# Optimization experiments

Hardware: AMD Instinct MI355X
Metric: run time of the kernel (lower is better)

Reference implementation:

```python
import jax, jax.numpy as jnp
import numpy as np

B, T, D = 2, 2048, 1024
N, K, H = 16, 8, 128  # q heads, kv heads, head_dim
G = N // K            # GQA group size
EPS = 1e-6
THETA = 1000000.0
SCALE = H ** -0.5
K_MASK = float(np.finfo(np.float32).min)


def rms_norm(x, scale):
    # RMSNorm over head_dim (last axis), computed in fp32 like the original
    dtype = x.dtype
    rms = jnp.sqrt(jnp.mean(x.astype(jnp.float32) ** 2, axis=-1, keepdims=True) + EPS)
    return (scale * x / rms).astype(dtype)


def positions_from_segment_ids(seg):
    t = jnp.arange(seg.shape[1], dtype=jnp.int32)[None, :]
    off = jnp.argmax(seg, axis=1, keepdims=True).astype(jnp.int32)
    rel = t - off
    return jnp.where(seg != 0, rel, jnp.int32(2 ** 30))


def rope_sin_cos(positions):
    frac = jnp.arange(0, H, 2, dtype=jnp.float32) / H
    inv_freq = 1.0 / (THETA ** frac)                    # [H/2]
    ang = positions.astype(jnp.float32)[..., None] * inv_freq  # [B,T,H/2]
    return jnp.sin(ang), jnp.cos(ang)


def apply_rope(x, sin, cos):
    # x: [B,T,heads,H]; sin/cos: [B,T,H/2]
    x1, x2 = x[..., : H // 2], x[..., H // 2:]
    s, c = sin[:, :, None, :], cos[:, :, None, :]
    return jnp.concatenate([x1 * c - x2 * s, x2 * c + x1 * s], axis=-1).astype(x.dtype)


def setup_inputs() -> dict:
    key = jax.random.key(0)
    ks = jax.random.split(key, 8)
    std = 0.02
    return {
        "x": jax.random.normal(ks[0], (B, T, D), dtype=jnp.float32),
        "segment_ids": jnp.ones((B, T), dtype=jnp.int32),
        "wq": jax.random.normal(ks[1], (D, N, H), dtype=jnp.float32) * std,
        "wk": jax.random.normal(ks[2], (D, K, H), dtype=jnp.float32) * std,
        "wv": jax.random.normal(ks[3], (D, K, H), dtype=jnp.float32) * std,
        "wo": jax.random.normal(ks[4], (N, H, D), dtype=jnp.float32) * std,
        "q_scale": jnp.ones((H,), dtype=jnp.float32),
        "k_scale": jnp.ones((H,), dtype=jnp.float32),
    }


def reference(x, segment_ids, wq, wk, wv, wo, q_scale, k_scale):
    # QKV projections + QK RMSNorm
    q = rms_norm(jnp.einsum('BTD,DNH->BTNH', x, wq), q_scale)  # [B,T,N,H]
    k = rms_norm(jnp.einsum('BSD,DKH->BSKH', x, wk), k_scale)  # [B,T,K,H]
    v = jnp.einsum('BSD,DKH->BSKH', x, wv)                     # [B,T,K,H]

    # RoPE using segment-relative positions
    pos = positions_from_segment_ids(segment_ids)  # [B,T] int32
    sin, cos = rope_sin_cos(pos)
    q = apply_rope(q, sin, cos)
    k = apply_rope(k, sin, cos)

    # GQA attention: [B,T,K,G,H] x [B,S,K,H] -> [B,T,S,K,G]
    qg = q.reshape(B, T, K, G, H)
    logits = jnp.einsum('BTKGH,BSKH->BTSKG', qg, k) * SCALE

    causal = pos[:, None, :] <= pos[:, :, None]                       # [B,T,S]
    segm = segment_ids[:, None, :] == segment_ids[:, :, None]         # [B,T,S]
    mask = (causal & segm)[:, :, :, None, None]
    logits = jnp.where(mask, logits, K_MASK)

    w = jax.nn.softmax(logits.astype(jnp.float32), axis=2).astype(logits.dtype)
    out = jnp.einsum('BTSKG,BSKH->BTKGH', w, v).reshape(B, T, N, H)
    return jnp.einsum('BTNH,NHD->BTD', out, wo)
```

## Files before the change

kernel.cpp:

```cpp
#include <hip/hip_runtime.h>
#include <hip/hip_bf16.h>


typedef unsigned short u16;
typedef __attribute__((ext_vector_type(8))) short s16x8;
typedef __attribute__((ext_vector_type(4))) float fp32x4;
typedef __attribute__((ext_vector_type(4))) u16 u16x4;

#define MFMA_BF16(a, b, c) __builtin_amdgcn_mfma_f32_16x16x32_bf16((a), (b), (c), 0, 0, 0)

static constexpr int Bq = 2, Tq = 2048, Dq = 1024, NHq = 16, KHq = 8, Hq = 128;
static constexpr float EPSq = 1e-6f;
static constexpr float S2q = 0.08838834764831845f * 1.4426950408889634f;
static constexpr float MAXq = 20.0f;
static constexpr float NEGHUGE = -3.0e38f;

__device__ __forceinline__ u16 f2b(float f) {
  __hip_bfloat16 h = __float2bfloat16(f);
  return *reinterpret_cast<u16*>(&h);
}

__device__ __forceinline__ void gload16(const u16* g, u16* lds_base) {
  __builtin_amdgcn_global_load_lds(
      (const __attribute__((address_space(1))) unsigned int*)(const void*)g,
      (__attribute__((address_space(3))) unsigned int*)(void*)lds_base, 16, 0, 0);
}


__global__ __launch_bounds__(256) void prep_kernel(
    const float* __restrict__ x, const float* __restrict__ wq,
    const float* __restrict__ wk, const float* __restrict__ wv,
    const float* __restrict__ wo, const int* __restrict__ seg,
    u16* __restrict__ xb, u16* __restrict__ wqkv_t, u16* __restrict__ wo_t,
    int* __restrict__ pos) {
  const int bid = blockIdx.x;
  const int tid = threadIdx.x;
  if (bid < 4096) {
    const int i = bid * 1024 + tid * 4;
    const float4 v = *reinterpret_cast<const float4*>(x + i);
    u16x4 o;
    o.x = f2b(v.x); o.y = f2b(v.y); o.z = f2b(v.z); o.w = f2b(v.w);
    *reinterpret_cast<u16x4*>(xb + i) = o;
    return;
  }
  __shared__ float tile[32][33];
  __shared__ int sv[256], si[256];
  const int tx = tid & 31, ty = tid >> 5;
  if (bid < 8192) {
    const int z = bid - 4096;
    const int r0 = (z & 31) * 32;
    const int c0 = (z >> 5) * 32;
    const float* src;
    int stride, coff;
    if (c0 < 2048)      { src = wq; stride = 2048; coff = c0; }
    else if (c0 < 3072) { src = wk; stride = 1024; coff = c0 - 2048; }
    else                { src = wv; stride = 1024; coff = c0 - 3072; }
#pragma unroll
    for (int j = 0; j < 32; j += 8)
      tile[ty + j][tx] = src[(long)(r0 + ty + j) * stride + (coff + tx)];
    __syncthreads();
#pragma unroll
    for (int j = 0; j < 32; j += 8)
      wqkv_t[(long)(c0 + ty + j) * 1024 + (r0 + tx)] = f2b(tile[tx][ty + j]);
    return;
  }
  if (bid < 10240) {
    const int z = bid - 8192;
    const int c0 = (z & 31) * 32;
    const int r0 = (z >> 5) * 32;
#pragma unroll
    for (int j = 0; j < 32; j += 8)
      tile[ty + j][tx] = wo[(long)(r0 + ty + j) * 1024 + (c0 + tx)];
    __syncthreads();
#pragma unroll
    for (int j = 0; j < 32; j += 8)
      wo_t[(long)(c0 + ty + j) * 2048 + (r0 + tx)] = f2b(tile[tx][ty + j]);
    return;
  }
  const int b = bid - 10240;
  const int* s = seg + b * Tq;
  int bestv = -2147483647 - 1, besti = 0x7fffffff;
  for (int t = tid; t < Tq; t += 256) {
    int v = s[t];
    if (v > bestv) { bestv = v; besti = t; }
  }
  sv[tid] = bestv; si[tid] = besti;
  __syncthreads();
  for (int k = 128; k > 0; k >>= 1) {
    if (tid < k) {
      int v2 = sv[tid + k], i2 = si[tid + k];
      if (v2 > sv[tid] || (v2 == sv[tid] && i2 < si[tid])) {
        sv[tid] = v2; si[tid] = i2;
      }
    }
    __syncthreads();
  }
  const int off = si[0];
  for (int t = tid; t < Tq; t += 256)
    pos[b * Tq + t] = (s[t] != 0) ? (t - off) : (1 << 30);
}


template <typename OutT, int BN>
__global__ __launch_bounds__(256) void gemm_bt_kernel(
    const u16* __restrict__ A, const u16* __restrict__ Bt, OutT* __restrict__ C,
    u16* __restrict__ vtout, int M, int N, int Kd) {
  constexpr int JT = BN / 32;
  __shared__ __align__(16) u16 As[128][64];
  __shared__ __align__(16) u16 Bs[BN][64];
  const int tid = threadIdx.x;
  const int wave = tid >> 6, lane = tid & 63;
  const int quad = lane >> 4, l16 = lane & 15;
  const int m0 = blockIdx.y * 128, n0 = blockIdx.x * BN;
  const int wm = (wave >> 1) * 64, wn = (wave & 1) * (BN / 2);
  const int row8 = lane >> 3;
  const int cgl = (lane & 7) ^ row8;

  const fp32x4 z4 = {0.f, 0.f, 0.f, 0.f};
  fp32x4 acc[4][JT];
#pragma unroll
  for (int i = 0; i < 4; ++i)
#pragma unroll
    for (int j = 0; j < JT; ++j) acc[i][j] = z4;

  for (int k0 = 0; k0 < Kd; k0 += 64) {
    __syncthreads();
#pragma unroll
    for (int jj = 0; jj < 4; ++jj) {
      const int R = wave * 32 + jj * 8;
      gload16(A + (size_t)(m0 + R + row8) * Kd + k0 + cgl * 8, &As[R][0]);
    }
    if constexpr (BN == 128) {
#pragma unroll
      for (int jj = 0; jj < 4; ++jj) {
        const int R = wave * 32 + jj * 8;
        gload16(Bt + (size_t)(n0 + R + row8) * Kd + k0 + cgl * 8, &Bs[R][0]);
      }
    } else {
#pragma unroll
      for (int jj = 0; jj < 2; ++jj) {
        const int R = wave * 16 + jj * 8;
        gload16(Bt + (size_t)(n0 + R + row8) * Kd + k0 + cgl * 8, &Bs[R][0]);
      }
    }
    __syncthreads();
#pragma unroll
    for (int kh = 0; kh < 2; ++kh) {
      s16x8 af[4], bfr[JT];
#pragma unroll
      for (int i = 0; i < 4; ++i)
        af[i] = *(const s16x8*)&As[wm + i * 16 + l16]
                               [((((kh << 2) | quad) ^ (l16 & 7)) << 3)];
#pragma unroll
      for (int j = 0; j < JT; ++j)
        bfr[j] = *(const s16x8*)&Bs[wn + j * 16 + l16]
                                [((((kh << 2) | quad) ^ (l16 & 7)) << 3)];
#pragma unroll
      for (int i = 0; i < 4; ++i)
#pragma unroll
        for (int j = 0; j < JT; ++j) acc[i][j] = MFMA_BF16(af[i], bfr[j], acc[i][j]);
    }
  }

  if constexpr (sizeof(OutT) == 2) {
    if (n0 >= 3072) {
      const int kv8 = (n0 - 3072) >> 7;
      const int bq = m0 >> 11;
      const size_t vbase = (size_t)(bq * KHq + kv8) * Hq * Tq;
#pragma unroll
      for (int i = 0; i < 4; ++i) {
        const int t = (m0 + wm + i * 16 + quad * 4) & 2047;
#pragma unroll
        for (int j = 0; j < JT; ++j) {
          const int h = wn + j * 16 + l16;
          u16x4 o;
#pragma unroll
          for (int r = 0; r < 4; ++r) o[r] = f2b(acc[i][j][r]);
          *reinterpret_cast<u16x4*>(&vtout[vbase + (size_t)h * Tq + t]) = o;
        }
      }
      return;
    }
  }
#pragma unroll
  for (int i = 0; i < 4; ++i) {
    const int row = m0 + wm + i * 16 + quad * 4;
#pragma unroll
    for (int j = 0; j < JT; ++j) {
      const int col = n0 + wn + j * 16 + l16;
#pragma unroll
      for (int r = 0; r < 4; ++r) {
        const float v = acc[i][j][r];
        if constexpr (sizeof(OutT) == 2)
          ((u16*)C)[(size_t)(row + r) * N + col] = f2b(v);
        else
          ((float*)C)[(size_t)(row + r) * N + col] = v;
      }
    }
  }
}


__global__ __launch_bounds__(256) void norm_rope_kernel(
    u16* __restrict__ qkv, const int* __restrict__ pos,
    const float* __restrict__ q_scale, const float* __restrict__ k_scale) {
  const int w = blockIdx.x * 4 + (threadIdx.x >> 6);
  const int lane = threadIdx.x & 63;
  const int bt = w / 24, head = w % 24;
  const bool isq = head < NHq;
  const int col = isq ? head * Hq : 2048 + (head - NHq) * Hq;
  u16* p = qkv + (size_t)bt * 4096 + col;
  const float e1 = (float)*reinterpret_cast<const __hip_bfloat16*>(&p[lane]);
  const float e2 = (float)*reinterpret_cast<const __hip_bfloat16*>(&p[lane + 64]);
  float ss = e1 * e1 + e2 * e2;
#pragma unroll
  for (int d = 1; d < 64; d <<= 1) ss += __shfl_xor(ss, d, 64);
  const float rinv = rsqrtf(ss * (1.0f / 128.0f) + EPSq);
  const float* sc = isq ? q_scale : k_scale;
  const float n1 = sc[lane] * e1 * rinv;
  const float n2 = sc[lane + 64] * e2 * rinv;
  const int P = pos[bt];
  const float inv_freq =
      __builtin_amdgcn_exp2f(-(float)lane * (19.931568569324174f / 64.0f));
  float r = (float)P * inv_freq * 0.15915494309189535f;
  r -= floorf(r);
  const float s = __builtin_amdgcn_sinf(r);
  const float c = __builtin_amdgcn_cosf(r);
  p[lane] = f2b(n1 * c - n2 * s);
  p[lane + 64] = f2b(n2 * c + n1 * s);
}


__global__ __launch_bounds__(256, 2) void flash_kernel(
    const u16* __restrict__ qkv, const u16* __restrict__ vt,
    const int* __restrict__ pos, const int* __restrict__ seg,
    u16* __restrict__ Obuf) {
  const int tid = threadIdx.x;
  const int w = tid >> 6;
  const int lane = tid & 63;
  const int quad = lane >> 4, l16 = lane & 15;
  const int g = blockIdx.x;
  const int b = g & 1;
  const int kv = (g >> 1) & 7;
  const int qh = kv * 2 + ((g >> 4) & 1);
  const int p = g >> 5;

  __shared__ __align__(16) u16 Ks[64][128];
  __shared__ __align__(16) u16 Vs[128][64];
  __shared__ __align__(16) u16 Ps[4][16][72];

  const u16* kbase = qkv + (size_t)(b * Tq) * 4096 + 2048 + kv * Hq;
  const u16* vbase = vt + (size_t)(b * KHq + kv) * Hq * Tq;
  const int krow_off = lane >> 4;
  const int vrow_off = lane >> 3;
  const fp32x4 z4 = {0.f, 0.f, 0.f, 0.f};

#pragma unroll
  for (int phase = 0; phase < 2; ++phase) {
    const int c = phase ? p : 31 - p;
    const int t0 = c * 64 + w * 16;
    const int nst = c + 1;

    s16x8 qf[4];
    {
      const u16* qrow = qkv + (size_t)(b * Tq + t0 + l16) * 4096 + qh * Hq;
#pragma unroll
      for (int ks = 0; ks < 4; ++ks)
        qf[ks] = *(const s16x8*)(qrow + ks * 32 + quad * 8);
    }
    int my_pos[4], my_seg[4];
#pragma unroll
    for (int i = 0; i < 4; ++i) {
      const int t = t0 + quad * 4 + i;
      my_pos[i] = pos[b * Tq + t];
      my_seg[i] = seg[b * Tq + t];
    }
    float l_i[4];
#pragma unroll
    for (int i = 0; i < 4; ++i) l_i[i] = 0.f;
    fp32x4 o_acc[8];
#pragma unroll
    for (int h = 0; h < 8; ++h) o_acc[h] = z4;

    for (int st = 0; st < nst; ++st) {
      const int s0 = st * 64;
      __syncthreads();
#pragma unroll
      for (int j = 0; j < 4; ++j) {
        const int R = w * 16 + j * 4;
        const int r = R + krow_off;
        const int cg = (lane & 15) ^ (r & 15);
        gload16(kbase + (size_t)(s0 + r) * 4096 + cg * 8, &Ks[R][0]);
      }
#pragma unroll
      for (int j = 0; j < 4; ++j) {
        const int R = w * 32 + j * 8;
        const int r = R + vrow_off;
        const int cg = (lane & 7) ^ (vrow_off & 7);
        gload16(vbase + (size_t)r * Tq + s0 + cg * 8, &Vs[R][0]);
      }
      __syncthreads();

      fp32x4 sc[4];
#pragma unroll
      for (int sub = 0; sub < 4; ++sub) sc[sub] = z4;
#pragma unroll
      for (int sub = 0; sub < 4; ++sub)
#pragma unroll
        for (int ks = 0; ks < 4; ++ks) {
          const s16x8 kf =
              *(const s16x8*)&Ks[sub * 16 + l16][((((ks << 2) | quad) ^ l16) << 3)];
          sc[sub] = MFMA_BF16(qf[ks], kf, sc[sub]);
        }

      if (st == nst - 1) {
        int spos[4], sseg[4];
#pragma unroll
        for (int sub = 0; sub < 4; ++sub) {
          const int s = s0 + sub * 16 + l16;
          spos[sub] = pos[b * Tq + s];
          sseg[sub] = seg[b * Tq + s];
        }
#pragma unroll
        for (int sub = 0; sub < 4; ++sub)
#pragma unroll
          for (int i = 0; i < 4; ++i) {
            const bool ok = (sseg[sub] == my_seg[i]) && (spos[sub] <= my_pos[i]);
            sc[sub][i] = ok ? sc[sub][i] * S2q - MAXq : NEGHUGE;
          }
      } else {
#pragma unroll
        for (int sub = 0; sub < 4; ++sub)
#pragma unroll
          for (int i = 0; i < 4; ++i) sc[sub][i] = sc[sub][i] * S2q - MAXq;
      }

#pragma unroll
      for (int i = 0; i < 4; ++i) {
        float rs = 0.f;
#pragma unroll
        for (int sub = 0; sub < 4; ++sub) {
          const float pv = __builtin_amdgcn_exp2f(sc[sub][i]);
          sc[sub][i] = pv;
          rs += pv;
        }
#pragma unroll
        for (int d = 1; d < 16; d <<= 1) rs += __shfl_xor(rs, d, 64);
        l_i[i] += rs;
      }

#pragma unroll
      for (int sub = 0; sub < 4; ++sub)
#pragma unroll
        for (int i = 0; i < 4; ++i)
          Ps[w][quad * 4 + i][sub * 16 + l16] = f2b(sc[sub][i]);
      asm volatile("s_waitcnt lgkmcnt(0)" ::: "memory");
      s16x8 pf[2];
#pragma unroll
      for (int kk = 0; kk < 2; ++kk)
        pf[kk] = *(const s16x8*)&Ps[w][l16][kk * 32 + quad * 8];

#pragma unroll
      for (int j = 0; j < 8; ++j)
#pragma unroll
        for (int kk = 0; kk < 2; ++kk) {
          const s16x8 vf =
              *(const s16x8*)&Vs[j * 16 + l16]
                             [((((kk << 2) | quad) ^ (l16 & 7)) << 3)];
          o_acc[j] = MFMA_BF16(pf[kk], vf, o_acc[j]);
        }
    }

#pragma unroll
    for (int i = 0; i < 4; ++i) l_i[i] = (l_i[i] > 0.f) ? 1.f / l_i[i] : 0.f;
#pragma unroll
    for (int j = 0; j < 8; ++j)
#pragma unroll
      for (int i = 0; i < 4; ++i) {
        const int t = t0 + quad * 4 + i;
        Obuf[(size_t)(b * Tq + t) * 2048 + qh * Hq + j * 16 + l16] =
            f2b(o_acc[j][i] * l_i[i]);
      }
  }
}


extern "C" void kernel_launch(void* const* d_in, const int* in_sizes, int n_in,
                              void* d_out, int out_size, void* d_ws, size_t ws_size,
                              hipStream_t stream) {
  const float* x = (const float*)d_in[0];
  const int* seg = (const int*)d_in[1];
  const float* wq = (const float*)d_in[2];
  const float* wk = (const float*)d_in[3];
  const float* wv = (const float*)d_in[4];
  const float* wo = (const float*)d_in[5];
  const float* q_scale = (const float*)d_in[6];
  const float* k_scale = (const float*)d_in[7];
  float* out = (float*)d_out;

  char* ws = (char*)d_ws;
  u16* xb = (u16*)(ws);
  u16* wqkv_t = (u16*)(ws + 8388608);
  u16* qkv = (u16*)(ws + 16777216);
  u16* vt = (u16*)(ws + 50331648);
  u16* wo_t = (u16*)(ws + 58720256);
  u16* Obuf = (u16*)(ws + 62914560);
  int* posb = (int*)(ws + 79691776);

  prep_kernel<<<10242, 256, 0, stream>>>(x, wq, wk, wv, wo, seg,
                                         xb, wqkv_t, wo_t, posb);

  gemm_bt_kernel<u16, 128><<<dim3(32, 32, 1), 256, 0, stream>>>(
      xb, wqkv_t, qkv, vt, 4096, 4096, 1024);

  norm_rope_kernel<<<24576, 256, 0, stream>>>(qkv, posb, q_scale, k_scale);

  flash_kernel<<<512, 256, 0, stream>>>(qkv, vt, posb, seg, Obuf);

  gemm_bt_kernel<float, 64><<<dim3(16, 32, 1), 256, 0, stream>>>(
      Obuf, wo_t, out, nullptr, 4096, 1024, 2048);
}
```

Measured before the change: 272.5 us.

## Fuse QK RMSNorm and RoPE into QKV GEMM epilogue; MFMA row sums

The QKV GEMM now gives each wave 32 rows by all 128 columns of a head, so the RMSNorm reduction and RoPE rotation run directly on the accumulators. This removes the separate norm_rope kernel launch and its read-modify-write pass over qkv. It also avoids the intermediate bf16 rounding before the norm. In the flash kernel, softmax row sums now come from an MFMA of the bf16 probabilities against a ones vector instead of shuffle reductions, which frees VALU work at the cost of two extra MFMAs per tile and denominators summed from rounded bf16 values.

```diff
diff --git a/kernel.cpp b/kernel.cpp
--- a/kernel.cpp
+++ b/kernel.cpp
@@ -101,133 +101,176 @@
 }
 
 
-template <typename OutT, int BN>
-__global__ __launch_bounds__(256) void gemm_bt_kernel(
-    const u16* __restrict__ A, const u16* __restrict__ Bt, OutT* __restrict__ C,
-    u16* __restrict__ vtout, int M, int N, int Kd) {
-  constexpr int JT = BN / 32;
+__global__ __launch_bounds__(256) void gemm_qkv_kernel(
+    const u16* __restrict__ A, const u16* __restrict__ Bt,
+    u16* __restrict__ qkv, u16* __restrict__ vt, const int* __restrict__ pos,
+    const float* __restrict__ q_scale, const float* __restrict__ k_scale) {
   __shared__ __align__(16) u16 As[128][64];
-  __shared__ __align__(16) u16 Bs[BN][64];
+  __shared__ __align__(16) u16 Bs[128][64];
   const int tid = threadIdx.x;
   const int wave = tid >> 6, lane = tid & 63;
   const int quad = lane >> 4, l16 = lane & 15;
-  const int m0 = blockIdx.y * 128, n0 = blockIdx.x * BN;
-  const int wm = (wave >> 1) * 64, wn = (wave & 1) * (BN / 2);
+  const int m0 = blockIdx.y * 128, n0 = blockIdx.x * 128;
   const int row8 = lane >> 3;
   const int cgl = (lane & 7) ^ row8;
 
   const fp32x4 z4 = {0.f, 0.f, 0.f, 0.f};
-  fp32x4 acc[4][JT];
-#pragma unroll
-  for (int i = 0; i < 4; ++i)
-#pragma unroll
-    for (int j = 0; j < JT; ++j) acc[i][j] = z4;
-
-  for (int k0 = 0; k0 < Kd; k0 += 64) {
+  fp32x4 acc[2][8];
+#pragma unroll
+  for (int i = 0; i < 2; ++i)
+#pragma unroll
+    for (int j = 0; j < 8; ++j) acc[i][j] = z4;
+
+  for (int k0 = 0; k0 < 1024; k0 += 64) {
     __syncthreads();
 #pragma unroll
     for (int jj = 0; jj < 4; ++jj) {
       const int R = wave * 32 + jj * 8;
-      gload16(A + (size_t)(m0 + R + row8) * Kd + k0 + cgl * 8, &As[R][0]);
-    }
-    if constexpr (BN == 128) {
-#pragma unroll
-      for (int jj = 0; jj < 4; ++jj) {
-        const int R = wave * 32 + jj * 8;
-        gload16(Bt + (size_t)(n0 + R + row8) * Kd + k0 + cgl * 8, &Bs[R][0]);
-      }
-    } else {
-#pragma unroll
-      for (int jj = 0; jj < 2; ++jj) {
-        const int R = wave * 16 + jj * 8;
-        gload16(Bt + (size_t)(n0 + R + row8) * Kd + k0 + cgl * 8, &Bs[R][0]);
-      }
+      gload16(A + (size_t)(m0 + R + row8) * 1024 + k0 + cgl * 8, &As[R][0]);
+      gload16(Bt + (size_t)(n0 + R + row8) * 1024 + k0 + cgl * 8, &Bs[R][0]);
     }
     __syncthreads();
 #pragma unroll
     for (int kh = 0; kh < 2; ++kh) {
-      s16x8 af[4], bfr[JT];
+      s16x8 af[2], bfr[8];
+#pragma unroll
+      for (int i = 0; i < 2; ++i)
+        af[i] = *(const s16x8*)&As[wave * 32 + i * 16 + l16]
+                               [((((kh << 2) | quad) ^ (l16 & 7)) << 3)];
+#pragma unroll
+      for (int j = 0; j < 8; ++j)
+        bfr[j] = *(const s16x8*)&Bs[j * 16 + l16]
+                                [((((kh << 2) | quad) ^ (l16 & 7)) << 3)];
+#pragma unroll
+      for (int i = 0; i < 2; ++i)
+#pragma unroll
+        for (int j = 0; j < 8; ++j) acc[i][j] = MFMA_BF16(af[i], bfr[j], acc[i][j]);
+    }
+  }
+
+  const int wrow = m0 + wave * 32;
+  if (n0 >= 3072) {
+    const int kv8 = (n0 - 3072) >> 7;
+    const int bq = wrow >> 11;
+    const size_t vbase = (size_t)(bq * KHq + kv8) * Hq * Tq;
+#pragma unroll
+    for (int i = 0; i < 2; ++i) {
+      const int t = (wrow + i * 16 + quad * 4) & 2047;
+#pragma unroll
+      for (int j = 0; j < 8; ++j) {
+        const int h = j * 16 + l16;
+        u16x4 o;
+#pragma unroll
+        for (int r = 0; r < 4; ++r) o[r] = f2b(acc[i][j][r]);
+        *reinterpret_cast<u16x4*>(&vt[vbase + (size_t)h * Tq + t]) = o;
+      }
+    }
+    return;
+  }
+  const float* scp = (n0 < 2048) ? q_scale : k_scale;
+  float scl[8];
+#pragma unroll
+  for (int j = 0; j < 8; ++j) scl[j] = scp[j * 16 + l16];
+  float invf[4];
+#pragma unroll
+  for (int jf = 0; jf < 4; ++jf)
+    invf[jf] = __builtin_amdgcn_exp2f(
+                   -(float)(jf * 16 + l16) * (19.931568569324174f / 64.0f)) *
+               0.15915494309189535f;
+#pragma unroll
+  for (int i = 0; i < 2; ++i) {
+    float ss[4] = {0.f, 0.f, 0.f, 0.f};
+#pragma unroll
+    for (int j = 0; j < 8; ++j)
+#pragma unroll
+      for (int r = 0; r < 4; ++r) ss[r] += acc[i][j][r] * acc[i][j][r];
+#pragma unroll
+    for (int d = 1; d < 16; d <<= 1)
+#pragma unroll
+      for (int r = 0; r < 4; ++r) ss[r] += __shfl_xor(ss[r], d, 64);
+#pragma unroll
+    for (int r = 0; r < 4; ++r) {
+      const int row = wrow + i * 16 + quad * 4 + r;
+      const float rinv = rsqrtf(ss[r] * (1.0f / 128.0f) + EPSq);
+      const float P = (float)pos[row];
+      u16* orow = qkv + (size_t)row * 4096 + n0;
+#pragma unroll
+      for (int jf = 0; jf < 4; ++jf) {
+        float rev = P * invf[jf];
+        rev -= floorf(rev);
+        const float s = __builtin_amdgcn_sinf(rev);
+        const float c = __builtin_amdgcn_cosf(rev);
+        const float a1 = acc[i][jf][r] * rinv * scl[jf];
+        const float a2 = acc[i][jf + 4][r] * rinv * scl[jf + 4];
+        orow[jf * 16 + l16] = f2b(a1 * c - a2 * s);
+        orow[(jf + 4) * 16 + l16] = f2b(a2 * c + a1 * s);
+      }
+    }
+  }
+}
+
+
+__global__ __launch_bounds__(256) void gemm_out_kernel(
+    const u16* __restrict__ A, const u16* __restrict__ Bt,
+    float* __restrict__ C) {
+  __shared__ __align__(16) u16 As[128][64];
+  __shared__ __align__(16) u16 Bs[64][64];
+  const int tid = threadIdx.x;
+  const int wave = tid >> 6, lane = tid & 63;
+  const int quad = lane >> 4, l16 = lane & 15;
+  const int m0 = blockIdx.y * 128, n0 = blockIdx.x * 64;
+  const int wm = (wave >> 1) * 64, wn = (wave & 1) * 32;
+  const int row8 = lane >> 3;
+  const int cgl = (lane & 7) ^ row8;
+
+  const fp32x4 z4 = {0.f, 0.f, 0.f, 0.f};
+  fp32x4 acc[4][2];
+#pragma unroll
+  for (int i = 0; i < 4; ++i)
+#pragma unroll
+    for (int j = 0; j < 2; ++j) acc[i][j] = z4;
+
+  for (int k0 = 0; k0 < 2048; k0 += 64) {
+    __syncthreads();
+#pragma unroll
+    for (int jj = 0; jj < 4; ++jj) {
+      const int R = wave * 32 + jj * 8;
+      gload16(A + (size_t)(m0 + R + row8) * 2048 + k0 + cgl * 8, &As[R][0]);
+    }
+#pragma unroll
+    for (int jj = 0; jj < 2; ++jj) {
+      const int R = wave * 16 + jj * 8;
+      gload16(Bt + (size_t)(n0 + R + row8) * 2048 + k0 + cgl * 8, &Bs[R][0]);
+    }
+    __syncthreads();
+#pragma unroll
+    for (int kh = 0; kh < 2; ++kh) {
+      s16x8 af[4], bfr[2];
 #pragma unroll
       for (int i = 0; i < 4; ++i)
         af[i] = *(const s16x8*)&As[wm + i * 16 + l16]
                                [((((kh << 2) | quad) ^ (l16 & 7)) << 3)];
 #pragma unroll
-      for (int j = 0; j < JT; ++j)
+      for (int j = 0; j < 2; ++j)
         bfr[j] = *(const s16x8*)&Bs[wn + j * 16 + l16]
                                 [((((kh << 2) | quad) ^ (l16 & 7)) << 3)];
 #pragma unroll
       for (int i = 0; i < 4; ++i)
 #pragma unroll
-        for (int j = 0; j < JT; ++j) acc[i][j] = MFMA_BF16(af[i], bfr[j], acc[i][j]);
-    }
-  }
-
-  if constexpr (sizeof(OutT) == 2) {
-    if (n0 >= 3072) {
-      const int kv8 = (n0 - 3072) >> 7;
-      const int bq = m0 >> 11;
-      const size_t vbase = (size_t)(bq * KHq + kv8) * Hq * Tq;
-#pragma unroll
-      for (int i = 0; i < 4; ++i) {
-        const int t = (m0 + wm + i * 16 + quad * 4) & 2047;
-#pragma unroll
-        for (int j = 0; j < JT; ++j) {
-          const int h = wn + j * 16 + l16;
-          u16x4 o;
-#pragma unroll
-          for (int r = 0; r < 4; ++r) o[r] = f2b(acc[i][j][r]);
-          *reinterpret_cast<u16x4*>(&vtout[vbase + (size_t)h * Tq + t]) = o;
-        }
-      }
-      return;
+        for (int j = 0; j < 2; ++j) acc[i][j] = MFMA_BF16(af[i], bfr[j], acc[i][j]);
     }
   }
 #pragma unroll
   for (int i = 0; i < 4; ++i) {
     const int row = m0 + wm + i * 16 + quad * 4;
 #pragma unroll
-    for (int j = 0; j < JT; ++j) {
+    for (int j = 0; j < 2; ++j) {
       const int col = n0 + wn + j * 16 + l16;
 #pragma unroll
-      for (int r = 0; r < 4; ++r) {
-        const float v = acc[i][j][r];
-        if constexpr (sizeof(OutT) == 2)
-          ((u16*)C)[(size_t)(row + r) * N + col] = f2b(v);
-        else
-          ((float*)C)[(size_t)(row + r) * N + col] = v;
-      }
-    }
-  }
-}
-
-
-__global__ __launch_bounds__(256) void norm_rope_kernel(
-    u16* __restrict__ qkv, const int* __restrict__ pos,
-    const float* __restrict__ q_scale, const float* __restrict__ k_scale) {
-  const int w = blockIdx.x * 4 + (threadIdx.x >> 6);
-  const int lane = threadIdx.x & 63;
-  const int bt = w / 24, head = w % 24;
-  const bool isq = head < NHq;
-  const int col = isq ? head * Hq : 2048 + (head - NHq) * Hq;
-  u16* p = qkv + (size_t)bt * 4096 + col;
-  const float e1 = (float)*reinterpret_cast<const __hip_bfloat16*>(&p[lane]);
-  const float e2 = (float)*reinterpret_cast<const __hip_bfloat16*>(&p[lane + 64]);
-  float ss = e1 * e1 + e2 * e2;
-#pragma unroll
-  for (int d = 1; d < 64; d <<= 1) ss += __shfl_xor(ss, d, 64);
-  const float rinv = rsqrtf(ss * (1.0f / 128.0f) + EPSq);
-  const float* sc = isq ? q_scale : k_scale;
-  const float n1 = sc[lane] * e1 * rinv;
-  const float n2 = sc[lane + 64] * e2 * rinv;
-  const int P = pos[bt];
-  const float inv_freq =
-      __builtin_amdgcn_exp2f(-(float)lane * (19.931568569324174f / 64.0f));
-  float r = (float)P * inv_freq * 0.15915494309189535f;
-  r -= floorf(r);
-  const float s = __builtin_amdgcn_sinf(r);
-  const float c = __builtin_amdgcn_cosf(r);
-  p[lane] = f2b(n1 * c - n2 * s);
-  p[lane + 64] = f2b(n2 * c + n1 * s);
+      for (int r = 0; r < 4; ++r)
+        C[(size_t)(row + r) * 1024 + col] = acc[i][j][r];
+    }
+  }
 }
 
 
@@ -254,6 +297,9 @@
   const int krow_off = lane >> 4;
   const int vrow_off = lane >> 3;
   const fp32x4 z4 = {0.f, 0.f, 0.f, 0.f};
+  const short one_bf = (short)0x3F80;
+  const s16x8 ones = {one_bf, one_bf, one_bf, one_bf,
+                      one_bf, one_bf, one_bf, one_bf};
 
 #pragma unroll
   for (int phase = 0; phase < 2; ++phase) {
@@ -275,9 +321,7 @@
       my_pos[i] = pos[b * Tq + t];
       my_seg[i] = seg[b * Tq + t];
     }
-    float l_i[4];
-#pragma unroll
-    for (int i = 0; i < 4; ++i) l_i[i] = 0.f;
+    fp32x4 l_acc = z4;
     fp32x4 o_acc[8];
 #pragma unroll
     for (int h = 0; h < 8; ++h) o_acc[h] = z4;
@@ -336,30 +380,19 @@
       }
 
 #pragma unroll
-      for (int i = 0; i < 4; ++i) {
-        float rs = 0.f;
-#pragma unroll
-        for (int sub = 0; sub < 4; ++sub) {
-          const float pv = __builtin_amdgcn_exp2f(sc[sub][i]);
-          sc[sub][i] = pv;
-          rs += pv;
-        }
-#pragma unroll
-        for (int d = 1; d < 16; d <<= 1) rs += __shfl_xor(rs, d, 64);
-        l_i[i] += rs;
-      }
-
-#pragma unroll
       for (int sub = 0; sub < 4; ++sub)
 #pragma unroll
         for (int i = 0; i < 4; ++i)
-          Ps[w][quad * 4 + i][sub * 16 + l16] = f2b(sc[sub][i]);
+          Ps[w][quad * 4 + i][sub * 16 + l16] =
+              f2b(__builtin_amdgcn_exp2f(sc[sub][i]));
       asm volatile("s_waitcnt lgkmcnt(0)" ::: "memory");
       s16x8 pf[2];
 #pragma unroll
       for (int kk = 0; kk < 2; ++kk)
         pf[kk] = *(const s16x8*)&Ps[w][l16][kk * 32 + quad * 8];
 
+      l_acc = MFMA_BF16(pf[0], ones, l_acc);
+      l_acc = MFMA_BF16(pf[1], ones, l_acc);
 #pragma unroll
       for (int j = 0; j < 8; ++j)
 #pragma unroll
@@ -371,15 +404,17 @@
         }
     }
 
-#pragma unroll
-    for (int i = 0; i < 4; ++i) l_i[i] = (l_i[i] > 0.f) ? 1.f / l_i[i] : 0.f;
+    float inv[4];
+#pragma unroll
+    for (int i = 0; i < 4; ++i)
+      inv[i] = (l_acc[i] > 0.f) ? 1.f / l_acc[i] : 0.f;
 #pragma unroll
     for (int j = 0; j < 8; ++j)
 #pragma unroll
       for (int i = 0; i < 4; ++i) {
         const int t = t0 + quad * 4 + i;
         Obuf[(size_t)(b * Tq + t) * 2048 + qh * Hq + j * 16 + l16] =
-            f2b(o_acc[j][i] * l_i[i]);
+            f2b(o_acc[j][i] * inv[i]);
       }
   }
 }
@@ -410,13 +445,10 @@
   prep_kernel<<<10242, 256, 0, stream>>>(x, wq, wk, wv, wo, seg,
                                          xb, wqkv_t, wo_t, posb);
 
-  gemm_bt_kernel<u16, 128><<<dim3(32, 32, 1), 256, 0, stream>>>(
-      xb, wqkv_t, qkv, vt, 4096, 4096, 1024);
-
-  norm_rope_kernel<<<24576, 256, 0, stream>>>(qkv, posb, q_scale, k_scale);
+  gemm_qkv_kernel<<<dim3(32, 32, 1), 256, 0, stream>>>(
+      xb, wqkv_t, qkv, vt, posb, q_scale, k_scale);
 
   flash_kernel<<<512, 256, 0, stream>>>(qkv, vt, posb, seg, Obuf);
 
-  gemm_bt_kernel<float, 64><<<dim3(16, 32, 1), 256, 0, stream>>>(
-      Obuf, wo_t, out, nullptr, 4096, 1024, 2048);
-}
+  gemm_out_kernel<<<dim3(16, 32, 1), 256, 0, stream>>>(Obuf, wo_t, out);
+}
```

Result: faster. 231.8 us (-14.9%).
